# Performance work log

Hardware: AMD Instinct MI355X
Metric: run time of the kernel (lower is better)

The kernel has to match this reference:

```python
import math
import jax, jax.numpy as jnp
import numpy as np

N_LAYER = 4
D = 192        # n_embd
NH = 4         # n_head
N = 3072       # n_neurons = n_embd * mlp_dim_mult // n_head
VOCAB = 256
BLOCK = 4096
EPS = 1e-5
B, T = 1, 1024


def get_freqs(n, theta=2.0 ** 16):
    t = np.arange(n, dtype=np.float32)
    q = np.floor(t / 2.0) * 2.0  # quantize(t, 2)
    return (1.0 / theta ** (q / n) / (2.0 * math.pi)).astype(np.float32)

_FREQS = jnp.asarray(get_freqs(N))  # [N]


def _ln(x):
    # LayerNorm over last dim, no affine (elementwise_affine=False)
    m = jnp.mean(x, axis=-1, keepdims=True)
    v = jnp.var(x, axis=-1, keepdims=True)
    return (x - m) / jnp.sqrt(v + EPS)


def _rope(x):
    # x: [B, nh, T, N]
    t = x.shape[2]
    phases = (jnp.arange(t, dtype=jnp.float32)[:, None] * _FREQS[None, :]) % 1.0 * (2.0 * math.pi)  # [T, N]
    x_even = x[..., 0::2]
    x_odd = x[..., 1::2]
    v_rot = jnp.stack((-x_odd, x_even), axis=-1).reshape(x.shape)
    return x * jnp.cos(phases) + v_rot * jnp.sin(phases)


def setup_inputs() -> dict:
    key = jax.random.key(0)
    ks = jax.random.split(key, 7)
    s = 0.02
    return {
        "idx": jax.random.randint(ks[0], (B, T), 0, VOCAB, dtype=jnp.int64)
        if jax.config.jax_enable_x64 else jax.random.randint(ks[0], (B, T), 0, VOCAB, dtype=jnp.int32),
        "decoder_x": jax.random.normal(ks[1], (NH, D, N), jnp.float32) * s,
        "decoder_y": jax.random.normal(ks[2], (NH, D, N), jnp.float32) * s,
        "encoder": jax.random.normal(ks[3], (NH * N, D), jnp.float32) * s,
        "embed": jax.random.normal(ks[4], (VOCAB, D), jnp.float32) * s,
        "pos_emb": jax.random.normal(ks[5], (BLOCK, D), jnp.float32) * s,
        "lm_head": jax.random.normal(ks[6], (D, VOCAB), jnp.float32) * s,
    }


def reference(idx, decoder_x, decoder_y, encoder, embed, pos_emb, lm_head):
    b, t = idx.shape
    x = embed[idx] + pos_emb[:t][None]          # [B, T, D]
    x = _ln(x)
    mask = jnp.tril(jnp.ones((t, t), jnp.float32), k=-1)  # strictly lower
    for _ in range(N_LAYER):
        # encoder-side sparsification: D -> N per head
        x_sparse = jax.nn.relu(jnp.einsum('btd,hdn->bhtn', x, decoder_x))  # [B,nh,T,N]
        qr = _rope(x_sparse)
        scores = jnp.einsum('bhtn,bhsn->bhts', qr, qr) * mask              # [B,nh,T,T]
        ykv = _ln(jnp.einsum('bhts,bsd->bhtd', scores, x))                 # [B,nh,T,D]
        y_sparse = jax.nn.relu(jnp.einsum('bhtd,hdn->bhtn', ykv, decoder_y))
        xy = x_sparse * y_sparse                                           # [B,nh,T,N]
        # [B,T,nh*N] @ [nh*N, D]
        ymlp = jnp.einsum('bhtn,hnd->btd', xy, encoder.reshape(NH, N, D))
        x = _ln(x + _ln(ymlp))
    logits = jnp.einsum('btd,dv->btv', x, lm_head)                         # [B,T,vocab]
    return logits
```

## Files before the change

### kernel.cpp

```cpp
#include <hip/hip_runtime.h>
#include <hip/hip_bf16.h>

using bf16 = __hip_bfloat16;

#define D_DIM   192
#define N_DIM   3072
#define NHEAD   4
#define T_SEQ   1024
#define HN      12288
#define NP2     1536
#define VOCABSZ 256
#define NLAYER  4
#define LN_EPS  1e-5f
#define TWO_PI  6.2831853071795864f

typedef __attribute__((ext_vector_type(8)))  short          s16x8;
typedef __attribute__((ext_vector_type(8)))  unsigned short u16x8;
typedef __attribute__((ext_vector_type(4)))  float          f32x4;
typedef __attribute__((ext_vector_type(16))) float          f32x16;

__device__ __forceinline__ float b2f(bf16 v) { return __bfloat162float(v); }
__device__ __forceinline__ float us2f(unsigned short u) {
    unsigned int x = ((unsigned int)u) << 16;
    return __builtin_bit_cast(float, x);
}
__device__ __forceinline__ unsigned short f2us(float f) {
    bf16 b = __float2bfloat16(f);
    return __builtin_bit_cast(unsigned short, b);
}

__global__ void fill_out(float* __restrict__ out, float val, int nelem) {
    int i = blockIdx.x * 256 + threadIdx.x;
    if (i < nelem) out[i] = val;
}

__global__ void t_cvt(const float* __restrict__ in, bf16* __restrict__ out,
                      int R, int C, long inZ, long outZ) {
    __shared__ float tile[64][65];
    in  += inZ  * blockIdx.z;
    out += outZ * blockIdx.z;
    const int tx = threadIdx.x & 63, ty = threadIdx.x >> 6;
    const int r0 = blockIdx.y * 64, c0 = blockIdx.x * 64;
    #pragma unroll
    for (int rr = 0; rr < 16; rr++) {
        int row = ty * 16 + rr;
        tile[row][tx] = in[(size_t)(r0 + row) * C + c0 + tx];
    }
    __syncthreads();
    #pragma unroll
    for (int rr = 0; rr < 16; rr++) {
        int row = ty * 16 + rr;
        out[(size_t)(c0 + row) * R + r0 + tx] = __float2bfloat16(tile[tx][row]);
    }
}

__device__ __forceinline__ void wave_sum2(float& s, float& ss) {
    #pragma unroll
    for (int off = 1; off < 64; off <<= 1) {
        s  += __shfl_xor(s,  off, 64);
        ss += __shfl_xor(ss, off, 64);
    }
}

__global__ void k_embed(const int* __restrict__ idx, const float* __restrict__ emb,
                        const float* __restrict__ pos, float* __restrict__ x) {
    int t = blockIdx.x, l = threadIdx.x;
    int tok = idx[t];
    const float* e = emb + tok * D_DIM;
    const float* p = pos + t * D_DIM;
    float v0 = e[l] + p[l], v1 = e[l + 64] + p[l + 64], v2 = e[l + 128] + p[l + 128];
    float s = v0 + v1 + v2, ss = v0 * v0 + v1 * v1 + v2 * v2;
    wave_sum2(s, ss);
    float m = s / D_DIM, r = rsqrtf(ss / D_DIM - m * m + LN_EPS);
    float* xr = x + t * D_DIM;
    xr[l] = (v0 - m) * r; xr[l + 64] = (v1 - m) * r; xr[l + 128] = (v2 - m) * r;
}

__global__ void k_ln(float* __restrict__ buf) {
    int l = threadIdx.x;
    float* row = buf + (size_t)blockIdx.x * D_DIM;
    float v0 = row[l], v1 = row[l + 64], v2 = row[l + 128];
    float s = v0 + v1 + v2, ss = v0 * v0 + v1 * v1 + v2 * v2;
    wave_sum2(s, ss);
    float m = s / D_DIM, r = rsqrtf(ss / D_DIM - m * m + LN_EPS);
    row[l] = (v0 - m) * r; row[l + 64] = (v1 - m) * r; row[l + 128] = (v2 - m) * r;
}

__global__ void k_ln2(float* __restrict__ buf, const float* __restrict__ P1) {
    int l = threadIdx.x;
    size_t off = (size_t)blockIdx.x * D_DIM;
    float* row = buf + off;
    const float* r1 = P1 + off;
    float v0 = row[l] + r1[l];
    float v1 = row[l + 64] + r1[l + 64];
    float v2 = row[l + 128] + r1[l + 128];
    float s = v0 + v1 + v2, ss = v0 * v0 + v1 * v1 + v2 * v2;
    wave_sum2(s, ss);
    float m = s / D_DIM, r = rsqrtf(ss / D_DIM - m * m + LN_EPS);
    row[l] = (v0 - m) * r; row[l + 64] = (v1 - m) * r; row[l + 128] = (v2 - m) * r;
}

__global__ void k_resid8(float* __restrict__ x, const float* __restrict__ P) {
    int l = threadIdx.x, t = blockIdx.x;
    float y0 = 0.f, y1 = 0.f, y2 = 0.f;
    #pragma unroll
    for (int p = 0; p < 8; p++) {
        const float* r = P + (size_t)p * T_SEQ * D_DIM + (size_t)t * D_DIM;
        y0 += r[l]; y1 += r[l + 64]; y2 += r[l + 128];
    }
    float* xr = x + (size_t)t * D_DIM;
    float s = y0 + y1 + y2, ss = y0 * y0 + y1 * y1 + y2 * y2;
    wave_sum2(s, ss);
    float m1 = s / D_DIM, r1 = rsqrtf(ss / D_DIM - m1 * m1 + LN_EPS);
    float v0 = xr[l] + (y0 - m1) * r1;
    float v1 = xr[l + 64] + (y1 - m1) * r1;
    float v2 = xr[l + 128] + (y2 - m1) * r1;
    s = v0 + v1 + v2; ss = v0 * v0 + v1 * v1 + v2 * v2;
    wave_sum2(s, ss);
    float m2 = s / D_DIM, r2 = rsqrtf(ss / D_DIM - m2 * m2 + LN_EPS);
    xr[l] = (v0 - m2) * r2; xr[l + 64] = (v1 - m2) * r2; xr[l + 128] = (v2 - m2) * r2;
}

__global__ void k_tables(ushort2* __restrict__ csT) {
    int gid = blockIdx.x * 256 + threadIdx.x;
    int t = gid / NP2, p = gid % NP2;
    float qf = (float)(2 * p);
    float f = exp2f(qf * (-16.0f / 3072.0f)) * (1.0f / (float)TWO_PI);
    float ph = fmodf((float)t * f, 1.0f) * (float)TWO_PI;
    ushort2 cs;
    cs.x = f2us(cosf(ph));
    cs.y = f2us(sinf(ph));
    csT[gid] = cs;
}

__launch_bounds__(256, 4)
__global__ void scores64(const bf16* __restrict__ qr, bf16* __restrict__ sc,
                         bf16* __restrict__ dbuf) {
    const int h  = blockIdx.z;
    const int kh = blockIdx.y;
    const int orig = blockIdx.x;
    const int L = (orig & 7) * 17 + (orig >> 3);
    int i = 0;
    while (((i + 1) * (i + 2)) >> 1 <= L) ++i;
    int j = L - ((i * (i + 1)) >> 1);
    const int t0 = i * 64, s0 = j * 64;
    const bool diag = (i == j);

    int arow = t0, brow = s0;
    if (kh == 1 && !diag) { arow = s0; brow = t0; }

    __shared__ short As[2][64][72];
    __shared__ short Bs[2][64][72];

    const int tid = threadIdx.x;
    const int lane = tid & 63, w = tid >> 6;
    const int wtm = (w >> 1) * 32, wtn = (w & 1) * 32;
    const int l31 = lane & 31, lhi = lane >> 5;
    const int r0 = tid >> 2;
    const int kq = (tid & 3) * 16;

    const int kBeg = kh * (N_DIM / 2);
    const bf16* gA = qr + (size_t)(arow + r0) * HN + h * N_DIM + kBeg + kq;
    const bf16* gB = qr + (size_t)(brow + r0) * HN + h * N_DIM + kBeg + kq;

    u16x8 pa0, pa1, pb0, pb1;
    u16x8 qa0, qa1, qb0, qb1;
    auto load0 = [&](int k0) {
        pa0 = *(const u16x8*)(gA + k0);
        pa1 = *(const u16x8*)(gA + k0 + 8);
        pb0 = *(const u16x8*)(gB + k0);
        pb1 = *(const u16x8*)(gB + k0 + 8);
    };
    auto load1 = [&](int k0) {
        qa0 = *(const u16x8*)(gA + k0);
        qa1 = *(const u16x8*)(gA + k0 + 8);
        qb0 = *(const u16x8*)(gB + k0);
        qb1 = *(const u16x8*)(gB + k0 + 8);
    };
    auto dep0 = [&](int buf) {
        *(u16x8*)&As[buf][r0][kq]     = pa0;
        *(u16x8*)&As[buf][r0][kq + 8] = pa1;
        *(u16x8*)&Bs[buf][r0][kq]     = pb0;
        *(u16x8*)&Bs[buf][r0][kq + 8] = pb1;
    };
    auto dep1 = [&](int buf) {
        *(u16x8*)&As[buf][r0][kq]     = qa0;
        *(u16x8*)&As[buf][r0][kq + 8] = qa1;
        *(u16x8*)&Bs[buf][r0][kq]     = qb0;
        *(u16x8*)&Bs[buf][r0][kq + 8] = qb1;
    };

    f32x16 acc;
    #pragma unroll
    for (int r = 0; r < 16; r++) acc[r] = 0.f;

    auto mfma_step = [&](int buf) {
        #pragma unroll
        for (int ks = 0; ks < 4; ks++) {
            s16x8 a = *(const s16x8*)&As[buf][wtm + l31][ks * 16 + lhi * 8];
            s16x8 b = *(const s16x8*)&Bs[buf][wtn + l31][ks * 16 + lhi * 8];
            acc = __builtin_amdgcn_mfma_f32_32x32x16_bf16(a, b, acc, 0, 0, 0);
        }
    };

    const int NIT = (N_DIM / 2) / 64;
    load0(0);
    load1(64);
    dep0(0);
    __syncthreads();

    for (int k = 0; k < NIT; k += 2) {
        if (k + 2 < NIT) load0((k + 2) * 64);
        mfma_step(0);
        if (k + 1 < NIT) dep1(1);
        __syncthreads();
        if (k + 1 < NIT) {
            if (k + 3 < NIT) load1((k + 3) * 64);
            mfma_step(1);
            if (k + 2 < NIT) dep0(0);
            __syncthreads();
        }
    }

    __syncthreads();
    short (*S)[72] = (short(*)[72])&As[0][0][0];
    const bool trS = (kh == 1) && !diag;
    #pragma unroll
    for (int r = 0; r < 16; r++) {
        int rr = wtm + (r & 3) + 8 * (r >> 2) + 4 * lhi;
        int cc = wtn + l31;
        float v = acc[r];
        if (diag && cc >= rr) v = 0.f;
        if (trS) S[cc][rr] = (short)f2us(v);
        else     S[rr][cc] = (short)f2us(v);
    }
    __syncthreads();
    if (kh == 1 && diag) {
        bf16* P = dbuf + (size_t)(h * 16 + i) * 4096;
        #pragma unroll
        for (int e = 0; e < 2; e++) {
            int idxe = tid + e * 256;
            int row = idxe >> 3, cg = (idxe & 7) * 8;
            u16x8 v = *(const u16x8*)&S[row][cg];
            *(u16x8*)(P + row * 64 + cg) = v;
        }
    } else {
        bf16* C = sc + (size_t)h * T_SEQ * T_SEQ;
        #pragma unroll
        for (int e = 0; e < 2; e++) {
            int idxe = tid + e * 256;
            int row = idxe >> 3, cg = (idxe & 7) * 8;
            u16x8 v = *(const u16x8*)&S[row][cg];
            *(u16x8*)(C + (size_t)(arow + row) * T_SEQ + brow + cg) = v;
        }
    }
}

__device__ __forceinline__ void stage_rope8(short* dst, const bf16* src,
                                            const ushort2* csP) {
    u16x8 v  = *(const u16x8*)src;
    u16x8 cs = *(const u16x8*)csP;
    u16x8 o;
    #pragma unroll
    for (int i = 0; i < 4; i++) {
        float e  = us2f(v[2 * i]), od = us2f(v[2 * i + 1]);
        float c  = us2f(cs[2 * i]), s = us2f(cs[2 * i + 1]);
        o[2 * i]     = f2us(e * c - od * s);
        o[2 * i + 1] = f2us(od * c + e * s);
    }
    *(u16x8*)dst = o;
}

__launch_bounds__(256)
__global__ void scores_fused(const bf16* __restrict__ xs,
                             const ushort2* __restrict__ csT,
                             bf16* __restrict__ sc) {
    const int h  = blockIdx.z;
    const int s0 = blockIdx.x * 64, t0 = blockIdx.y * 64;
    if (s0 > t0) return;
    __shared__ short As[64][40];
    __shared__ short Bs[64][40];
    const int tid  = threadIdx.x;
    const int srow = tid >> 2, kq = (tid & 3) * 8;
    const int lane = tid & 63, w = tid >> 6, qd = lane >> 4, lc = lane & 15;
    const int tA = t0 + srow, tB = s0 + srow;
    const bf16* gA = xs + (size_t)tA * HN + h * N_DIM + kq;
    const bf16* gB = xs + (size_t)tB * HN + h * N_DIM + kq;
    const ushort2* cA = csT + (size_t)tA * NP2 + (kq >> 1);
    const ushort2* cB = csT + (size_t)tB * NP2 + (kq >> 1);
    f32x4 acc[4] = {{0.f,0.f,0.f,0.f},{0.f,0.f,0.f,0.f},
                    {0.f,0.f,0.f,0.f},{0.f,0.f,0.f,0.f}};
    for (int k0 = 0; k0 < N_DIM; k0 += 32) {
        stage_rope8(&As[srow][kq], gA + k0, cA + (k0 >> 1));
        stage_rope8(&Bs[srow][kq], gB + k0, cB + (k0 >> 1));
        __syncthreads();
        s16x8 a = *(const s16x8*)&As[w * 16 + lc][qd * 8];
        #pragma unroll
        for (int j = 0; j < 4; j++) {
            s16x8 b = *(const s16x8*)&Bs[j * 16 + lc][qd * 8];
            acc[j] = __builtin_amdgcn_mfma_f32_16x16x32_bf16(a, b, acc[j], 0, 0, 0);
        }
        __syncthreads();
    }
    bf16* C = sc + (size_t)h * T_SEQ * T_SEQ;
    const bool diag = (s0 == t0);
    const int tbase = t0 + w * 16 + qd * 4;
    #pragma unroll
    for (int j = 0; j < 4; j++) {
        int s = s0 + j * 16 + lc;
        #pragma unroll
        for (int r = 0; r < 4; r++) {
            int t = tbase + r;
            C[(size_t)t * T_SEQ + s] =
                __float2bfloat16((!diag || s < t) ? acc[j][r] : 0.f);
        }
    }
}

template <int EPI, bool WQR>
__launch_bounds__(256)
__global__ void dgemm128(const float* __restrict__ A, const bf16* __restrict__ Bt,
                         bf16* __restrict__ xs, bf16* __restrict__ qr,
                         const ushort2* __restrict__ csT) {
    __shared__ __align__(16) short pool[2 * 2 * 128 * 40];
    short (*As)[128][40] = (short(*)[128][40])pool;
    short (*Bs)[128][40] = (short(*)[128][40])(pool + 2 * 128 * 40);

    const int tid = threadIdx.x;
    const int lane = tid & 63, w = tid >> 6, qd = lane >> 4, lc = lane & 15;
    const int wtm = (w >> 1) * 64, wtn = (w & 1) * 64;
    const int n0 = blockIdx.x * 128, m0 = blockIdx.y * 128;
    if constexpr (EPI == 2) A += (size_t)(n0 / N_DIM) * T_SEQ * D_DIM;

    const int r0 = tid >> 2, r1 = r0 + 64;
    const int kq = (tid & 3) * 8;

    const float* gA = A  + kq;
    const bf16*  gB = Bt + kq;

    float4 fa00, fa01, fa02, fa03, fa10, fa11, fa12, fa13;
    u16x8 pb00, pb01, pb10, pb11;
    auto load0 = [&](int k0) {
        const float* a0 = gA + (size_t)(m0 + r0) * D_DIM + k0;
        const float* a1 = gA + (size_t)(m0 + r1) * D_DIM + k0;
        fa00 = *(const float4*)a0; fa01 = *(const float4*)(a0 + 4);
        fa02 = *(const float4*)a1; fa03 = *(const float4*)(a1 + 4);
        pb00 = *(const u16x8*)(gB + (size_t)(n0 + r0) * D_DIM + k0);
        pb01 = *(const u16x8*)(gB + (size_t)(n0 + r1) * D_DIM + k0);
    };
    auto load1 = [&](int k0) {
        const float* a0 = gA + (size_t)(m0 + r0) * D_DIM + k0;
        const float* a1 = gA + (size_t)(m0 + r1) * D_DIM + k0;
        fa10 = *(const float4*)a0; fa11 = *(const float4*)(a0 + 4);
        fa12 = *(const float4*)a1; fa13 = *(const float4*)(a1 + 4);
        pb10 = *(const u16x8*)(gB + (size_t)(n0 + r0) * D_DIM + k0);
        pb11 = *(const u16x8*)(gB + (size_t)(n0 + r1) * D_DIM + k0);
    };
    auto dep0 = [&](int buf) {
        u16x8 o0, o1;
        o0[0] = f2us(fa00.x); o0[1] = f2us(fa00.y); o0[2] = f2us(fa00.z); o0[3] = f2us(fa00.w);
        o0[4] = f2us(fa01.x); o0[5] = f2us(fa01.y); o0[6] = f2us(fa01.z); o0[7] = f2us(fa01.w);
        o1[0] = f2us(fa02.x); o1[1] = f2us(fa02.y); o1[2] = f2us(fa02.z); o1[3] = f2us(fa02.w);
        o1[4] = f2us(fa03.x); o1[5] = f2us(fa03.y); o1[6] = f2us(fa03.z); o1[7] = f2us(fa03.w);
        *(u16x8*)&As[buf][r0][kq] = o0;
        *(u16x8*)&As[buf][r1][kq] = o1;
        *(u16x8*)&Bs[buf][r0][kq] = pb00;
        *(u16x8*)&Bs[buf][r1][kq] = pb01;
    };
    auto dep1 = [&](int buf) {
        u16x8 o0, o1;
        o0[0] = f2us(fa10.x); o0[1] = f2us(fa10.y); o0[2] = f2us(fa10.z); o0[3] = f2us(fa10.w);
        o0[4] = f2us(fa11.x); o0[5] = f2us(fa11.y); o0[6] = f2us(fa11.z); o0[7] = f2us(fa11.w);
        o1[0] = f2us(fa12.x); o1[1] = f2us(fa12.y); o1[2] = f2us(fa12.z); o1[3] = f2us(fa12.w);
        o1[4] = f2us(fa13.x); o1[5] = f2us(fa13.y); o1[6] = f2us(fa13.z); o1[7] = f2us(fa13.w);
        *(u16x8*)&As[buf][r0][kq] = o0;
        *(u16x8*)&As[buf][r1][kq] = o1;
        *(u16x8*)&Bs[buf][r0][kq] = pb10;
        *(u16x8*)&Bs[buf][r1][kq] = pb11;
    };

    f32x4 acc[4][4] = {};
    auto mfma_step = [&](int buf) {
        s16x8 a[4], b[4];
        #pragma unroll
        for (int m = 0; m < 4; m++) a[m] = *(const s16x8*)&As[buf][wtm + m * 16 + lc][qd * 8];
        #pragma unroll
        for (int n = 0; n < 4; n++) b[n] = *(const s16x8*)&Bs[buf][wtn + n * 16 + lc][qd * 8];
        #pragma unroll
        for (int m = 0; m < 4; m++)
            #pragma unroll
            for (int n = 0; n < 4; n++)
                acc[m][n] = __builtin_amdgcn_mfma_f32_16x16x32_bf16(a[m], b[n], acc[m][n], 0, 0, 0);
    };

    const int NIT = D_DIM / 32;
    load0(0);
    load1(32);
    dep0(0);
    __syncthreads();
    for (int k = 0; k < NIT; k += 2) {
        if (k + 2 < NIT) load0((k + 2) * 32);
        mfma_step(0);
        if (k + 1 < NIT) dep1(1);
        __syncthreads();
        if (k + 1 < NIT) {
            if (k + 3 < NIT) load1((k + 3) * 32);
            mfma_step(1);
            if (k + 2 < NIT) dep0(0);
            __syncthreads();
        }
    }

    short (*S)[136] = (short(*)[136])pool;
    #pragma unroll
    for (int m = 0; m < 4; m++) {
        #pragma unroll
        for (int r = 0; r < 4; r++) {
            int tl = wtm + m * 16 + qd * 4 + r;
            #pragma unroll
            for (int n = 0; n < 4; n++) {
                int cl = wtn + n * 16 + lc;
                S[tl][cl] = (short)f2us(fmaxf(acc[m][n][r], 0.f));
            }
        }
    }
    __syncthreads();
    #pragma unroll
    for (int e = 0; e < 8; e++) {
        int idxe = tid + e * 256;
        int row = idxe >> 4, cg = idxe & 15;
        u16x8 v = *(const u16x8*)&S[row][cg * 8];
        int t = m0 + row, ngg = n0 + cg * 8;
        size_t ci = (size_t)t * HN + ngg;
        if constexpr (EPI == 1) {
            *(u16x8*)(xs + ci) = v;
            if constexpr (WQR) {
                int p0 = (ngg % N_DIM) >> 1;
                u16x8 cs8 = *(const u16x8*)&csT[(size_t)t * NP2 + p0];
                u16x8 o;
                #pragma unroll
                for (int q = 0; q < 4; q++) {
                    float ev = us2f(v[2 * q]), ov = us2f(v[2 * q + 1]);
                    float c = us2f(cs8[2 * q]), s = us2f(cs8[2 * q + 1]);
                    o[2 * q]     = f2us(ev * c - ov * s);
                    o[2 * q + 1] = f2us(ov * c + ev * s);
                }
                *(u16x8*)(qr + ci) = o;
            }
        } else {
            u16x8 g = *(const u16x8*)(xs + ci);
            u16x8 o;
            #pragma unroll
            for (int q = 0; q < 8; q++) o[q] = f2us(us2f(g[q]) * us2f(v[q]));
            *(u16x8*)(xs + ci) = o;
        }
    }
}

template <typename TA, int MODE>
__launch_bounds__(256)
__global__ void mfma_gemm(const TA* __restrict__ A, const bf16* __restrict__ Bt,
                          float* __restrict__ C, const bf16* __restrict__ aux,
                          int K, int kSeg, int lda, int ldb, int ldc,
                          long aZ, long bZ, long cZ) {
    constexpr bool DUAL = (MODE == 1);
    constexpr int TILES = DUAL ? 6 : 4;
    __shared__ __align__(16) short pool[TILES * 64 * 72];
    short (*As)[64][72] = (short(*)[64][72])pool;
    short (*Bs)[64][72] = (short(*)[64][72])(pool + 2 * 64 * 72);
    short (*Ms)[64][72] = (short(*)[64][72])(pool + 4 * 64 * 72);

    const int z = blockIdx.z;
    const int tid = threadIdx.x;
    const int n0 = blockIdx.x * 64, m0 = blockIdx.y * 64;
    const int srow = tid >> 2, sk = (tid & 3) * 16;
    const int lane = tid & 63, w = tid >> 6;
    const int l31 = lane & 31, lhi = lane >> 5;
    const int wm = (w >> 1) * 32, wn = (w & 1) * 32;

    int kBeg, kEnd, zh = 0;
    if constexpr (MODE == 1) {
        zh = z >> 1;
        const int seg = z & 1;
        A += aZ * zh;
        C += cZ * zh + bZ * seg;
        const int kc = (m0 + 64 < K) ? m0 + 64 : K;
        const int half0 = ((kc + 127) >> 7) << 6;
        kBeg = seg ? half0 : 0;
        kEnd = seg ? kc : half0;
    } else if constexpr (MODE == 2) {
        A += aZ * z; Bt += bZ * z; C += cZ * z;
        kBeg = z * kSeg; kEnd = kBeg + kSeg;
    } else if constexpr (MODE == 3) {
        A += aZ * z; Bt += bZ * z; C += cZ * z;
        kBeg = 0; kEnd = (m0 + 64 < K) ? m0 + 64 : K;
    } else {
        A += aZ * z; Bt += bZ * z; C += cZ * z;
        kBeg = 0; kEnd = K;
    }

    const TA*   ga = A  + (size_t)(m0 + srow) * lda + sk;
    const bf16* gb = Bt + (size_t)(n0 + srow) * ldb + sk;

    auto msrc = [&](int k0) -> const bf16* {
        if (k0 == m0)
            return aux + (size_t)(zh * 16 + (m0 >> 6)) * 4096
                       + (size_t)srow * 64 + sk;
        return (const bf16*)A + (size_t)(k0 + srow) * lda + m0 + sk;
    };

    float4 f00, f01, f02, f03, f10, f11, f12, f13;
    u16x8 pa00, pa01, pa10, pa11, pb00, pb01, pb10, pb11;
    u16x8 pm00, pm01, pm10, pm11;
    auto load0 = [&](int k0) {
        if constexpr (__is_same(TA, float)) {
            f00 = *(const float4*)(ga + k0);
            f01 = *(const float4*)(ga + k0 + 4);
            f02 = *(const float4*)(ga + k0 + 8);
            f03 = *(const float4*)(ga + k0 + 12);
        } else {
            pa00 = *(const u16x8*)(ga + k0);
            pa01 = *(const u16x8*)(ga + k0 + 8);
        }
        pb00 = *(const u16x8*)(gb + k0);
        pb01 = *(const u16x8*)(gb + k0 + 8);
        if constexpr (DUAL) {
            const bf16* ms = msrc(k0);
            pm00 = *(const u16x8*)ms;
            pm01 = *(const u16x8*)(ms + 8);
        }
    };
    auto load1 = [&](int k0) {
        if constexpr (__is_same(TA, float)) {
            f10 = *(const float4*)(ga + k0);
            f11 = *(const float4*)(ga + k0 + 4);
            f12 = *(const float4*)(ga + k0 + 8);
            f13 = *(const float4*)(ga + k0 + 12);
        } else {
            pa10 = *(const u16x8*)(ga + k0);
            pa11 = *(const u16x8*)(ga + k0 + 8);
        }
        pb10 = *(const u16x8*)(gb + k0);
        pb11 = *(const u16x8*)(gb + k0 + 8);
        if constexpr (DUAL) {
            const bf16* ms = msrc(k0);
            pm10 = *(const u16x8*)ms;
            pm11 = *(const u16x8*)(ms + 8);
        }
    };
    auto dep0 = [&](int buf) {
        if constexpr (__is_same(TA, float)) {
            u16x8 o0, o1;
            o0[0] = f2us(f00.x); o0[1] = f2us(f00.y); o0[2] = f2us(f00.z); o0[3] = f2us(f00.w);
            o0[4] = f2us(f01.x); o0[5] = f2us(f01.y); o0[6] = f2us(f01.z); o0[7] = f2us(f01.w);
            o1[0] = f2us(f02.x); o1[1] = f2us(f02.y); o1[2] = f2us(f02.z); o1[3] = f2us(f02.w);
            o1[4] = f2us(f03.x); o1[5] = f2us(f03.y); o1[6] = f2us(f03.z); o1[7] = f2us(f03.w);
            *(u16x8*)&As[buf][srow][sk]     = o0;
            *(u16x8*)&As[buf][srow][sk + 8] = o1;
        } else {
            *(u16x8*)&As[buf][srow][sk]     = pa00;
            *(u16x8*)&As[buf][srow][sk + 8] = pa01;
        }
        *(u16x8*)&Bs[buf][srow][sk]     = pb00;
        *(u16x8*)&Bs[buf][srow][sk + 8] = pb01;
        if constexpr (DUAL) {
            *(u16x8*)&Ms[buf][srow][sk]     = pm00;
            *(u16x8*)&Ms[buf][srow][sk + 8] = pm01;
        }
    };
    auto dep1 = [&](int buf) {
        if constexpr (__is_same(TA, float)) {
            u16x8 o0, o1;
            o0[0] = f2us(f10.x); o0[1] = f2us(f10.y); o0[2] = f2us(f10.z); o0[3] = f2us(f10.w);
            o0[4] = f2us(f11.x); o0[5] = f2us(f11.y); o0[6] = f2us(f11.z); o0[7] = f2us(f11.w);
            o1[0] = f2us(f12.x); o1[1] = f2us(f12.y); o1[2] = f2us(f12.z); o1[3] = f2us(f12.w);
            o1[4] = f2us(f13.x); o1[5] = f2us(f13.y); o1[6] = f2us(f13.z); o1[7] = f2us(f13.w);
            *(u16x8*)&As[buf][srow][sk]     = o0;
            *(u16x8*)&As[buf][srow][sk + 8] = o1;
        } else {
            *(u16x8*)&As[buf][srow][sk]     = pa10;
            *(u16x8*)&As[buf][srow][sk + 8] = pa11;
        }
        *(u16x8*)&Bs[buf][srow][sk]     = pb10;
        *(u16x8*)&Bs[buf][srow][sk + 8] = pb11;
        if constexpr (DUAL) {
            *(u16x8*)&Ms[buf][srow][sk]     = pm10;
            *(u16x8*)&Ms[buf][srow][sk + 8] = pm11;
        }
    };

    f32x16 acc;
    #pragma unroll
    for (int r = 0; r < 16; r++) acc[r] = 0.f;

    auto mfma_step = [&](int buf) {
        #pragma unroll
        for (int ks = 0; ks < 4; ks++) {
            s16x8 a = *(const s16x8*)&As[buf][wm + l31][ks * 16 + lhi * 8];
            s16x8 b = *(const s16x8*)&Bs[buf][wn + l31][ks * 16 + lhi * 8];
            acc = __builtin_amdgcn_mfma_f32_32x32x16_bf16(a, b, acc, 0, 0, 0);
            if constexpr (DUAL) {
                s16x8 m2 = *(const s16x8*)&Ms[buf][wm + l31][ks * 16 + lhi * 8];
                acc = __builtin_amdgcn_mfma_f32_32x32x16_bf16(m2, b, acc, 0, 0, 0);
            }
        }
    };

    const int NIT = (kEnd - kBeg) >> 6;
    load0(kBeg);
    load1(kBeg + 64);
    dep0(0);
    __syncthreads();

    for (int k = 0; k < NIT; k += 2) {
        if (k + 2 < NIT) load0(kBeg + (k + 2) * 64);
        mfma_step(0);
        if (k + 1 < NIT) dep1(1);
        __syncthreads();
        if (k + 1 < NIT) {
            if (k + 3 < NIT) load1(kBeg + (k + 3) * 64);
            mfma_step(1);
            if (k + 2 < NIT) dep0(0);
            __syncthreads();
        }
    }

    #pragma unroll
    for (int r = 0; r < 16; r++) {
        int row = m0 + wm + (r & 3) + 8 * (r >> 2) + 4 * lhi;
        int col = n0 + wn + l31;
        C[(size_t)row * ldc + col] = acc[r];
    }
}

extern "C" void kernel_launch(void* const* d_in, const int* in_sizes, int n_in,
                              void* d_out, int out_size, void* d_ws, size_t ws_size,
                              hipStream_t stream) {
    const int*   idx   = (const int*)  d_in[0];
    const float* dec_x = (const float*)d_in[1];
    const float* dec_y = (const float*)d_in[2];
    const float* enc   = (const float*)d_in[3];
    const float* emb   = (const float*)d_in[4];
    const float* pose  = (const float*)d_in[5];
    const float* lmh   = (const float*)d_in[6];
    float* out = (float*)d_out;

    char* wp = (char*)d_ws;
    float*   x    = (float*)wp;              wp += (size_t)T_SEQ * D_DIM * 4;
    bf16*    xs   = (bf16*)wp;               wp += (size_t)T_SEQ * HN * 2;
    ushort2* csT  = (ushort2*)wp;            wp += (size_t)T_SEQ * NP2 * 4;
    bf16*    sc   = (bf16*)wp;               wp += (size_t)NHEAD * T_SEQ * T_SEQ * 2;
    float*   ykv  = (float*)wp;              wp += (size_t)NHEAD * T_SEQ * D_DIM * 4;
    float*   ymlp = (float*)wp;              wp += (size_t)T_SEQ * D_DIM * 4;
    bf16*    xT   = (bf16*)wp;               wp += (size_t)D_DIM * T_SEQ * 2;
    bf16*    wX   = (bf16*)wp;               wp += (size_t)NHEAD * N_DIM * D_DIM * 2;
    bf16*    wY   = (bf16*)wp;               wp += (size_t)NHEAD * N_DIM * D_DIM * 2;
    bf16*    wE   = (bf16*)wp;               wp += (size_t)D_DIM * HN * 2;
    bf16*    wL   = (bf16*)wp;               wp += (size_t)VOCABSZ * D_DIM * 2;
    const size_t BASE_NEED = (size_t)(wp - (char*)d_ws);
    bf16*    qr   = (bf16*)wp;
    const size_t FULL_NEED = BASE_NEED + (size_t)T_SEQ * HN * 2;
    float* ymlpP = (float*)sc;
    bf16*  dbuf  = (bf16*)ymlp;

    if (ws_size < BASE_NEED) {
        fill_out<<<(out_size + 255) / 256, 256, 0, stream>>>(out, (float)ws_size, out_size);
        return;
    }
    const bool USE_QR = (ws_size >= FULL_NEED);

    t_cvt<<<dim3(48, 3, 4), 256, 0, stream>>>(dec_x, wX, D_DIM, N_DIM,
                                              (long)D_DIM * N_DIM, (long)N_DIM * D_DIM);
    t_cvt<<<dim3(48, 3, 4), 256, 0, stream>>>(dec_y, wY, D_DIM, N_DIM,
                                              (long)D_DIM * N_DIM, (long)N_DIM * D_DIM);
    t_cvt<<<dim3(3, 192, 1), 256, 0, stream>>>(enc, wE, HN, D_DIM, 0L, 0L);
    t_cvt<<<dim3(4, 3, 1), 256, 0, stream>>>(lmh, wL, D_DIM, VOCABSZ, 0L, 0L);

    k_tables<<<(T_SEQ * NP2) / 256, 256, 0, stream>>>(csT);
    k_embed<<<T_SEQ, 64, 0, stream>>>(idx, emb, pose, x);

    for (int l = 0; l < NLAYER; ++l) {
        t_cvt<<<dim3(3, 16, 1), 256, 0, stream>>>(x, xT, T_SEQ, D_DIM, 0L, 0L);
        if (USE_QR) {
            dgemm128<1, true><<<dim3(96, 8), 256, 0, stream>>>(x, wX, xs, qr, csT);
            scores64<<<dim3(136, 2, NHEAD), 256, 0, stream>>>(qr, sc, dbuf);
            long segZ = (long)((float*)qr - ykv);
            mfma_gemm<bf16, 1><<<dim3(3, 16, NHEAD * 2), 256, 0, stream>>>(
                sc, xT, ykv, dbuf, T_SEQ, 0, T_SEQ, T_SEQ, D_DIM,
                (long)T_SEQ * T_SEQ, segZ, (long)T_SEQ * D_DIM);
            k_ln2<<<NHEAD * T_SEQ, 64, 0, stream>>>(ykv, (const float*)qr);
        } else {
            dgemm128<1, false><<<dim3(96, 8), 256, 0, stream>>>(x, wX, xs, qr, csT);
            scores_fused<<<dim3(16, 16, NHEAD), 256, 0, stream>>>(xs, csT, sc);
            mfma_gemm<bf16, 3><<<dim3(3, 16, NHEAD), 256, 0, stream>>>(
                sc, xT, ykv, nullptr, T_SEQ, 0, T_SEQ, T_SEQ, D_DIM,
                (long)T_SEQ * T_SEQ, 0L, (long)T_SEQ * D_DIM);
            k_ln<<<NHEAD * T_SEQ, 64, 0, stream>>>(ykv);
        }
        dgemm128<2, false><<<dim3(96, 8), 256, 0, stream>>>(
            (const float*)ykv, wY, xs, nullptr, nullptr);
        mfma_gemm<bf16, 2><<<dim3(3, 16, 8), 256, 0, stream>>>(
            xs, wE, ymlpP, nullptr, HN, HN / 8, HN, HN, D_DIM,
            0L, 0L, (long)T_SEQ * D_DIM);
        k_resid8<<<T_SEQ, 64, 0, stream>>>(x, ymlpP);
    }

    mfma_gemm<float, 0><<<dim3(4, 16, 1), 256, 0, stream>>>(
        x, wL, out, nullptr, D_DIM, 0, D_DIM, D_DIM, VOCABSZ, 0L, 0L, 0L);
}
```

Baseline: 516.6 us.

## Feed bf16 activations to dgemm128, use 32x32 MFMA, widen encoder split-K

The layernorm kernels (embed, ln2, resid) now also write bf16 copies of their outputs, and dgemm128 reads these bf16 activations directly instead of loading fp32 and converting each tile. The dgemm inner loop switches from 16x16x32 MFMA tiles to 32x32x16 MFMA with four f32x16 accumulators, with a matching epilogue mapping. In the full-workspace path the encoder GEMM split-K goes from 8 to 16 slabs, written into the qr region, to add parallelism. The cost is extra bf16 stores, more partial-sum traffic in the residual reduction, and workspace aliasing that must not collide.

```diff
diff --git a/kernel.cpp b/kernel.cpp
--- a/kernel.cpp
+++ b/kernel.cpp
@@ -63,7 +63,8 @@
 }
 
 __global__ void k_embed(const int* __restrict__ idx, const float* __restrict__ emb,
-                        const float* __restrict__ pos, float* __restrict__ x) {
+                        const float* __restrict__ pos, float* __restrict__ x,
+                        bf16* __restrict__ xb) {
     int t = blockIdx.x, l = threadIdx.x;
     int tok = idx[t];
     const float* e = emb + tok * D_DIM;
@@ -73,7 +74,12 @@
     wave_sum2(s, ss);
     float m = s / D_DIM, r = rsqrtf(ss / D_DIM - m * m + LN_EPS);
     float* xr = x + t * D_DIM;
-    xr[l] = (v0 - m) * r; xr[l + 64] = (v1 - m) * r; xr[l + 128] = (v2 - m) * r;
+    bf16*  xo = xb + (size_t)t * D_DIM;
+    float o0 = (v0 - m) * r, o1 = (v1 - m) * r, o2 = (v2 - m) * r;
+    xr[l] = o0; xr[l + 64] = o1; xr[l + 128] = o2;
+    xo[l] = __float2bfloat16(o0);
+    xo[l + 64] = __float2bfloat16(o1);
+    xo[l + 128] = __float2bfloat16(o2);
 }
 
 __global__ void k_ln(float* __restrict__ buf) {
@@ -86,25 +92,31 @@
     row[l] = (v0 - m) * r; row[l + 64] = (v1 - m) * r; row[l + 128] = (v2 - m) * r;
 }
 
-__global__ void k_ln2(float* __restrict__ buf, const float* __restrict__ P1) {
+__global__ void k_ln2b(const float* __restrict__ P0, const float* __restrict__ P1,
+                       bf16* __restrict__ outb) {
     int l = threadIdx.x;
     size_t off = (size_t)blockIdx.x * D_DIM;
-    float* row = buf + off;
+    const float* r0 = P0 + off;
     const float* r1 = P1 + off;
-    float v0 = row[l] + r1[l];
-    float v1 = row[l + 64] + r1[l + 64];
-    float v2 = row[l + 128] + r1[l + 128];
+    float v0 = r0[l] + r1[l];
+    float v1 = r0[l + 64] + r1[l + 64];
+    float v2 = r0[l + 128] + r1[l + 128];
     float s = v0 + v1 + v2, ss = v0 * v0 + v1 * v1 + v2 * v2;
     wave_sum2(s, ss);
     float m = s / D_DIM, r = rsqrtf(ss / D_DIM - m * m + LN_EPS);
-    row[l] = (v0 - m) * r; row[l + 64] = (v1 - m) * r; row[l + 128] = (v2 - m) * r;
-}
-
-__global__ void k_resid8(float* __restrict__ x, const float* __restrict__ P) {
+    bf16* o = outb + off;
+    o[l]       = __float2bfloat16((v0 - m) * r);
+    o[l + 64]  = __float2bfloat16((v1 - m) * r);
+    o[l + 128] = __float2bfloat16((v2 - m) * r);
+}
+
+template <int NSLAB>
+__global__ void k_resid(float* __restrict__ x, const float* __restrict__ P,
+                        bf16* __restrict__ xb) {
     int l = threadIdx.x, t = blockIdx.x;
     float y0 = 0.f, y1 = 0.f, y2 = 0.f;
     #pragma unroll
-    for (int p = 0; p < 8; p++) {
+    for (int p = 0; p < NSLAB; p++) {
         const float* r = P + (size_t)p * T_SEQ * D_DIM + (size_t)t * D_DIM;
         y0 += r[l]; y1 += r[l + 64]; y2 += r[l + 128];
     }
@@ -118,7 +130,12 @@
     s = v0 + v1 + v2; ss = v0 * v0 + v1 * v1 + v2 * v2;
     wave_sum2(s, ss);
     float m2 = s / D_DIM, r2 = rsqrtf(ss / D_DIM - m2 * m2 + LN_EPS);
-    xr[l] = (v0 - m2) * r2; xr[l + 64] = (v1 - m2) * r2; xr[l + 128] = (v2 - m2) * r2;
+    float o0 = (v0 - m2) * r2, o1 = (v1 - m2) * r2, o2 = (v2 - m2) * r2;
+    xr[l] = o0; xr[l + 64] = o1; xr[l + 128] = o2;
+    bf16* xo = xb + (size_t)t * D_DIM;
+    xo[l] = __float2bfloat16(o0);
+    xo[l + 64] = __float2bfloat16(o1);
+    xo[l + 128] = __float2bfloat16(o2);
 }
 
 __global__ void k_tables(ushort2* __restrict__ csT) {
@@ -317,9 +334,9 @@
     }
 }
 
-template <int EPI, bool WQR>
+template <int EPI, bool WQR, typename TA>
 __launch_bounds__(256)
-__global__ void dgemm128(const float* __restrict__ A, const bf16* __restrict__ Bt,
+__global__ void dgemm128(const TA* __restrict__ A, const bf16* __restrict__ Bt,
                          bf16* __restrict__ xs, bf16* __restrict__ qr,
                          const ushort2* __restrict__ csT) {
     __shared__ __align__(16) short pool[2 * 2 * 128 * 40];
@@ -327,7 +344,8 @@
     short (*Bs)[128][40] = (short(*)[128][40])(pool + 2 * 128 * 40);
 
     const int tid = threadIdx.x;
-    const int lane = tid & 63, w = tid >> 6, qd = lane >> 4, lc = lane & 15;
+    const int lane = tid & 63, w = tid >> 6;
+    const int l31 = lane & 31, lhi = lane >> 5;
     const int wtm = (w >> 1) * 64, wtn = (w & 1) * 64;
     const int n0 = blockIdx.x * 128, m0 = blockIdx.y * 128;
     if constexpr (EPI == 2) A += (size_t)(n0 / N_DIM) * T_SEQ * D_DIM;
@@ -335,62 +353,87 @@
     const int r0 = tid >> 2, r1 = r0 + 64;
     const int kq = (tid & 3) * 8;
 
-    const float* gA = A  + kq;
-    const bf16*  gB = Bt + kq;
+    const TA*   gA = A  + kq;
+    const bf16* gB = Bt + kq;
 
     float4 fa00, fa01, fa02, fa03, fa10, fa11, fa12, fa13;
+    u16x8 ba00, ba01, ba10, ba11;
     u16x8 pb00, pb01, pb10, pb11;
     auto load0 = [&](int k0) {
-        const float* a0 = gA + (size_t)(m0 + r0) * D_DIM + k0;
-        const float* a1 = gA + (size_t)(m0 + r1) * D_DIM + k0;
-        fa00 = *(const float4*)a0; fa01 = *(const float4*)(a0 + 4);
-        fa02 = *(const float4*)a1; fa03 = *(const float4*)(a1 + 4);
+        if constexpr (__is_same(TA, float)) {
+            const TA* a0 = gA + (size_t)(m0 + r0) * D_DIM + k0;
+            const TA* a1 = gA + (size_t)(m0 + r1) * D_DIM + k0;
+            fa00 = *(const float4*)a0; fa01 = *(const float4*)(a0 + 4);
+            fa02 = *(const float4*)a1; fa03 = *(const float4*)(a1 + 4);
+        } else {
+            ba00 = *(const u16x8*)(gA + (size_t)(m0 + r0) * D_DIM + k0);
+            ba01 = *(const u16x8*)(gA + (size_t)(m0 + r1) * D_DIM + k0);
+        }
         pb00 = *(const u16x8*)(gB + (size_t)(n0 + r0) * D_DIM + k0);
         pb01 = *(const u16x8*)(gB + (size_t)(n0 + r1) * D_DIM + k0);
     };
     auto load1 = [&](int k0) {
-        const float* a0 = gA + (size_t)(m0 + r0) * D_DIM + k0;
-        const float* a1 = gA + (size_t)(m0 + r1) * D_DIM + k0;
-        fa10 = *(const float4*)a0; fa11 = *(const float4*)(a0 + 4);
-        fa12 = *(const float4*)a1; fa13 = *(const float4*)(a1 + 4);
+        if constexpr (__is_same(TA, float)) {
+            const TA* a0 = gA + (size_t)(m0 + r0) * D_DIM + k0;
+            const TA* a1 = gA + (size_t)(m0 + r1) * D_DIM + k0;
+            fa10 = *(const float4*)a0; fa11 = *(const float4*)(a0 + 4);
+            fa12 = *(const float4*)a1; fa13 = *(const float4*)(a1 + 4);
+        } else {
+            ba10 = *(const u16x8*)(gA + (size_t)(m0 + r0) * D_DIM + k0);
+            ba11 = *(const u16x8*)(gA + (size_t)(m0 + r1) * D_DIM + k0);
+        }
         pb10 = *(const u16x8*)(gB + (size_t)(n0 + r0) * D_DIM + k0);
         pb11 = *(const u16x8*)(gB + (size_t)(n0 + r1) * D_DIM + k0);
     };
     auto dep0 = [&](int buf) {
-        u16x8 o0, o1;
-        o0[0] = f2us(fa00.x); o0[1] = f2us(fa00.y); o0[2] = f2us(fa00.z); o0[3] = f2us(fa00.w);
-        o0[4] = f2us(fa01.x); o0[5] = f2us(fa01.y); o0[6] = f2us(fa01.z); o0[7] = f2us(fa01.w);
-        o1[0] = f2us(fa02.x); o1[1] = f2us(fa02.y); o1[2] = f2us(fa02.z); o1[3] = f2us(fa02.w);
-        o1[4] = f2us(fa03.x); o1[5] = f2us(fa03.y); o1[6] = f2us(fa03.z); o1[7] = f2us(fa03.w);
-        *(u16x8*)&As[buf][r0][kq] = o0;
-        *(u16x8*)&As[buf][r1][kq] = o1;
+        if constexpr (__is_same(TA, float)) {
+            u16x8 o0, o1;
+            o0[0] = f2us(fa00.x); o0[1] = f2us(fa00.y); o0[2] = f2us(fa00.z); o0[3] = f2us(fa00.w);
+            o0[4] = f2us(fa01.x); o0[5] = f2us(fa01.y); o0[6] = f2us(fa01.z); o0[7] = f2us(fa01.w);
+            o1[0] = f2us(fa02.x); o1[1] = f2us(fa02.y); o1[2] = f2us(fa02.z); o1[3] = f2us(fa02.w);
+            o1[4] = f2us(fa03.x); o1[5] = f2us(fa03.y); o1[6] = f2us(fa03.z); o1[7] = f2us(fa03.w);
+            *(u16x8*)&As[buf][r0][kq] = o0;
+            *(u16x8*)&As[buf][r1][kq] = o1;
+        } else {
+            *(u16x8*)&As[buf][r0][kq] = ba00;
+            *(u16x8*)&As[buf][r1][kq] = ba01;
+        }
         *(u16x8*)&Bs[buf][r0][kq] = pb00;
         *(u16x8*)&Bs[buf][r1][kq] = pb01;
     };
     auto dep1 = [&](int buf) {
-        u16x8 o0, o1;
-        o0[0] = f2us(fa10.x); o0[1] = f2us(fa10.y); o0[2] = f2us(fa10.z); o0[3] = f2us(fa10.w);
-        o0[4] = f2us(fa11.x); o0[5] = f2us(fa11.y); o0[6] = f2us(fa11.z); o0[7] = f2us(fa11.w);
-        o1[0] = f2us(fa12.x); o1[1] = f2us(fa12.y); o1[2] = f2us(fa12.z); o1[3] = f2us(fa12.w);
-        o1[4] = f2us(fa13.x); o1[5] = f2us(fa13.y); o1[6] = f2us(fa13.z); o1[7] = f2us(fa13.w);
-        *(u16x8*)&As[buf][r0][kq] = o0;
-        *(u16x8*)&As[buf][r1][kq] = o1;
+        if constexpr (__is_same(TA, float)) {
+            u16x8 o0, o1;
+            o0[0] = f2us(fa10.x); o0[1] = f2us(fa10.y); o0[2] = f2us(fa10.z); o0[3] = f2us(fa10.w);
+            o0[4] = f2us(fa11.x); o0[5] = f2us(fa11.y); o0[6] = f2us(fa11.z); o0[7] = f2us(fa11.w);
+            o1[0] = f2us(fa12.x); o1[1] = f2us(fa12.y); o1[2] = f2us(fa12.z); o1[3] = f2us(fa12.w);
+            o1[4] = f2us(fa13.x); o1[5] = f2us(fa13.y); o1[6] = f2us(fa13.z); o1[7] = f2us(fa13.w);
+            *(u16x8*)&As[buf][r0][kq] = o0;
+            *(u16x8*)&As[buf][r1][kq] = o1;
+        } else {
+            *(u16x8*)&As[buf][r0][kq] = ba10;
+            *(u16x8*)&As[buf][r1][kq] = ba11;
+        }
         *(u16x8*)&Bs[buf][r0][kq] = pb10;
         *(u16x8*)&Bs[buf][r1][kq] = pb11;
     };
 
-    f32x4 acc[4][4] = {};
+    f32x16 acc00, acc01, acc10, acc11;
+    #pragma unroll
+    for (int r = 0; r < 16; r++) { acc00[r] = 0.f; acc01[r] = 0.f; acc10[r] = 0.f; acc11[r] = 0.f; }
+
     auto mfma_step = [&](int buf) {
-        s16x8 a[4], b[4];
         #pragma unroll
-        for (int m = 0; m < 4; m++) a[m] = *(const s16x8*)&As[buf][wtm + m * 16 + lc][qd * 8];
-        #pragma unroll
-        for (int n = 0; n < 4; n++) b[n] = *(const s16x8*)&Bs[buf][wtn + n * 16 + lc][qd * 8];
-        #pragma unroll
-        for (int m = 0; m < 4; m++)
-            #pragma unroll
-            for (int n = 0; n < 4; n++)
-                acc[m][n] = __builtin_amdgcn_mfma_f32_16x16x32_bf16(a[m], b[n], acc[m][n], 0, 0, 0);
+        for (int ks = 0; ks < 2; ks++) {
+            s16x8 a0 = *(const s16x8*)&As[buf][wtm + l31][ks * 16 + lhi * 8];
+            s16x8 a1 = *(const s16x8*)&As[buf][wtm + 32 + l31][ks * 16 + lhi * 8];
+            s16x8 b0 = *(const s16x8*)&Bs[buf][wtn + l31][ks * 16 + lhi * 8];
+            s16x8 b1 = *(const s16x8*)&Bs[buf][wtn + 32 + l31][ks * 16 + lhi * 8];
+            acc00 = __builtin_amdgcn_mfma_f32_32x32x16_bf16(a0, b0, acc00, 0, 0, 0);
+            acc01 = __builtin_amdgcn_mfma_f32_32x32x16_bf16(a0, b1, acc01, 0, 0, 0);
+            acc10 = __builtin_amdgcn_mfma_f32_32x32x16_bf16(a1, b0, acc10, 0, 0, 0);
+            acc11 = __builtin_amdgcn_mfma_f32_32x32x16_bf16(a1, b1, acc11, 0, 0, 0);
+        }
     };
 
     const int NIT = D_DIM / 32;
@@ -413,16 +456,12 @@
 
     short (*S)[136] = (short(*)[136])pool;
     #pragma unroll
-    for (int m = 0; m < 4; m++) {
-        #pragma unroll
-        for (int r = 0; r < 4; r++) {
-            int tl = wtm + m * 16 + qd * 4 + r;
-            #pragma unroll
-            for (int n = 0; n < 4; n++) {
-                int cl = wtn + n * 16 + lc;
-                S[tl][cl] = (short)f2us(fmaxf(acc[m][n][r], 0.f));
-            }
-        }
+    for (int r = 0; r < 16; r++) {
+        int rb = (r & 3) + 8 * (r >> 2) + 4 * lhi;
+        S[wtm + rb     ][wtn + l31     ] = (short)f2us(fmaxf(acc00[r], 0.f));
+        S[wtm + rb     ][wtn + 32 + l31] = (short)f2us(fmaxf(acc01[r], 0.f));
+        S[wtm + 32 + rb][wtn + l31     ] = (short)f2us(fmaxf(acc10[r], 0.f));
+        S[wtm + 32 + rb][wtn + 32 + l31] = (short)f2us(fmaxf(acc11[r], 0.f));
     }
     __syncthreads();
     #pragma unroll
@@ -660,7 +699,6 @@
     const size_t BASE_NEED = (size_t)(wp - (char*)d_ws);
     bf16*    qr   = (bf16*)wp;
     const size_t FULL_NEED = BASE_NEED + (size_t)T_SEQ * HN * 2;
-    float* ymlpP = (float*)sc;
     bf16*  dbuf  = (bf16*)ymlp;
 
     if (ws_size < BASE_NEED) {
@@ -668,6 +706,14 @@
         return;
     }
     const bool USE_QR = (ws_size >= FULL_NEED);
+
+    bf16*  xb_main = (bf16*)sc;
+    bf16*  xb_fb   = (bf16*)ymlp;
+    float* ymlpP16 = (float*)qr;
+    bf16*  ykvb    = (bf16*)((char*)qr + (size_t)16 * T_SEQ * D_DIM * 4);
+    float* ymlpP8  = (float*)sc;
+
+    bf16* xb = USE_QR ? xb_main : xb_fb;
 
     t_cvt<<<dim3(48, 3, 4), 256, 0, stream>>>(dec_x, wX, D_DIM, N_DIM,
                                               (long)D_DIM * N_DIM, (long)N_DIM * D_DIM);
@@ -677,32 +723,38 @@
     t_cvt<<<dim3(4, 3, 1), 256, 0, stream>>>(lmh, wL, D_DIM, VOCABSZ, 0L, 0L);
 
     k_tables<<<(T_SEQ * NP2) / 256, 256, 0, stream>>>(csT);
-    k_embed<<<T_SEQ, 64, 0, stream>>>(idx, emb, pose, x);
+    k_embed<<<T_SEQ, 64, 0, stream>>>(idx, emb, pose, x, xb);
 
     for (int l = 0; l < NLAYER; ++l) {
         t_cvt<<<dim3(3, 16, 1), 256, 0, stream>>>(x, xT, T_SEQ, D_DIM, 0L, 0L);
         if (USE_QR) {
-            dgemm128<1, true><<<dim3(96, 8), 256, 0, stream>>>(x, wX, xs, qr, csT);
+            dgemm128<1, true, bf16><<<dim3(96, 8), 256, 0, stream>>>(xb, wX, xs, qr, csT);
             scores64<<<dim3(136, 2, NHEAD), 256, 0, stream>>>(qr, sc, dbuf);
             long segZ = (long)((float*)qr - ykv);
             mfma_gemm<bf16, 1><<<dim3(3, 16, NHEAD * 2), 256, 0, stream>>>(
                 sc, xT, ykv, dbuf, T_SEQ, 0, T_SEQ, T_SEQ, D_DIM,
                 (long)T_SEQ * T_SEQ, segZ, (long)T_SEQ * D_DIM);
-            k_ln2<<<NHEAD * T_SEQ, 64, 0, stream>>>(ykv, (const float*)qr);
-        } else {
-            dgemm128<1, false><<<dim3(96, 8), 256, 0, stream>>>(x, wX, xs, qr, csT);
+            k_ln2b<<<NHEAD * T_SEQ, 64, 0, stream>>>(ykv, (const float*)qr, ykvb);
+            dgemm128<2, false, bf16><<<dim3(96, 8), 256, 0, stream>>>(
+                ykvb, wY, xs, nullptr, nullptr);
+            mfma_gemm<bf16, 2><<<dim3(3, 16, 16), 256, 0, stream>>>(
+                xs, wE, ymlpP16, nullptr, HN, HN / 16, HN, HN, D_DIM,
+                0L, 0L, (long)T_SEQ * D_DIM);
+            k_resid<16><<<T_SEQ, 64, 0, stream>>>(x, ymlpP16, xb);
+        } else {
+            dgemm128<1, false, bf16><<<dim3(96, 8), 256, 0, stream>>>(xb, wX, xs, qr, csT);
             scores_fused<<<dim3(16, 16, NHEAD), 256, 0, stream>>>(xs, csT, sc);
             mfma_gemm<bf16, 3><<<dim3(3, 16, NHEAD), 256, 0, stream>>>(
                 sc, xT, ykv, nullptr, T_SEQ, 0, T_SEQ, T_SEQ, D_DIM,
                 (long)T_SEQ * T_SEQ, 0L, (long)T_SEQ * D_DIM);
             k_ln<<<NHEAD * T_SEQ, 64, 0, stream>>>(ykv);
-        }
-        dgemm128<2, false><<<dim3(96, 8), 256, 0, stream>>>(
-            (const float*)ykv, wY, xs, nullptr, nullptr);
-        mfma_gemm<bf16, 2><<<dim3(3, 16, 8), 256, 0, stream>>>(
-            xs, wE, ymlpP, nullptr, HN, HN / 8, HN, HN, D_DIM,
-            0L, 0L, (long)T_SEQ * D_DIM);
-        k_resid8<<<T_SEQ, 64, 0, stream>>>(x, ymlpP);
+            dgemm128<2, false, float><<<dim3(96, 8), 256, 0, stream>>>(
+                ykv, wY, xs, nullptr, nullptr);
+            mfma_gemm<bf16, 2><<<dim3(3, 16, 8), 256, 0, stream>>>(
+                xs, wE, ymlpP8, nullptr, HN, HN / 8, HN, HN, D_DIM,
+                0L, 0L, (long)T_SEQ * D_DIM);
+            k_resid<8><<<T_SEQ, 64, 0, stream>>>(x, ymlpP8, xb);
+        }
     }
 
     mfma_gemm<float, 0><<<dim3(4, 16, 1), 256, 0, stream>>>(
```

After: 519.2 us. Within noise of the previous version (+0.5%).
